# Performance work log

Hardware: AMD Instinct MI355X
Metric: run time of the kernel (lower is better)

The kernel has to match this reference:

```python
import jax, jax.numpy as jnp
import numpy as np

B, L, V, DM, NL, NH, DH, FF, K = 32, 128, 30522, 768, 12, 12, 64, 3072, 9
T = L - 1  # [CLS] stripped


def setup_inputs() -> dict:
    key = jax.random.key(0)
    ks = jax.random.split(key, 24)
    w = lambda k, s: jax.random.normal(k, s, jnp.float32) * 0.02
    u = lambda k, s: jax.random.uniform(k, s, jnp.float32, -0.1, 0.1)  # torchcrf init
    return dict(
        input_ids=jax.random.randint(ks[0], (B, L), 0, V, jnp.int32),
        attention_mask=jnp.ones((B, L), jnp.int32),
        token_type_ids=jnp.zeros((B, L), jnp.int32),
        y_true=jax.random.randint(ks[1], (B, T), 0, K, jnp.int32),
        word_emb=w(ks[2], (V, DM)), pos_emb=w(ks[3], (L, DM)), type_emb=w(ks[4], (2, DM)),
        emb_g=jnp.ones((DM,), jnp.float32), emb_b=jnp.zeros((DM,), jnp.float32),
        Wq=w(ks[5], (NL, DM, DM)), bq=jnp.zeros((NL, DM), jnp.float32),
        Wk=w(ks[6], (NL, DM, DM)), bk=jnp.zeros((NL, DM), jnp.float32),
        Wv=w(ks[7], (NL, DM, DM)), bv=jnp.zeros((NL, DM), jnp.float32),
        Wo=w(ks[8], (NL, DM, DM)), bo=jnp.zeros((NL, DM), jnp.float32),
        ln1_g=jnp.ones((NL, DM), jnp.float32), ln1_b=jnp.zeros((NL, DM), jnp.float32),
        W1=w(ks[9], (NL, DM, FF)), b1=jnp.zeros((NL, FF), jnp.float32),
        W2=w(ks[10], (NL, FF, DM)), b2=jnp.zeros((NL, DM), jnp.float32),
        ln2_g=jnp.ones((NL, DM), jnp.float32), ln2_b=jnp.zeros((NL, DM), jnp.float32),
        head_W=w(ks[11], (DM, K)), head_b=jnp.zeros((K,), jnp.float32),
        crf_start=u(ks[12], (K,)), crf_end=u(ks[13], (K,)), crf_trans=u(ks[14], (K, K)),
    )


def _ln(x, g, b):
    m = jnp.mean(x, -1, keepdims=True)
    v = jnp.var(x, -1, keepdims=True)
    return (x - m) * jax.lax.rsqrt(v + 1e-12) * g + b


def reference(input_ids, attention_mask, token_type_ids, y_true, word_emb, pos_emb,
              type_emb, emb_g, emb_b, Wq, bq, Wk, bk, Wv, bv, Wo, bo, ln1_g, ln1_b,
              W1, b1, W2, b2, ln2_g, ln2_b, head_W, head_b, crf_start, crf_end, crf_trans):
    # ----- BERT-base encoder -----
    x = word_emb[input_ids] + pos_emb[None, :, :] + type_emb[token_type_ids]
    x = _ln(x, emb_g, emb_b)
    bias = (1.0 - attention_mask.astype(jnp.float32))[:, None, None, :] * -1e9
    scale = 1.0 / jnp.sqrt(jnp.float32(DH))

    def layer(h, p):
        wq, bq_, wk, bk_, wv, bv_, wo, bo_, g1, gb1, w1, b1_, w2, b2_, g2, gb2 = p
        q = (h @ wq + bq_).reshape(B, L, NH, DH)
        k = (h @ wk + bk_).reshape(B, L, NH, DH)
        v = (h @ wv + bv_).reshape(B, L, NH, DH)
        s = jnp.einsum('bqhd,bkhd->bhqk', q, k) * scale + bias
        a = jax.nn.softmax(s, axis=-1)
        ctx = jnp.einsum('bhqk,bkhd->bqhd', a, v).reshape(B, L, DM)
        h = _ln(h + ctx @ wo + bo_, g1, gb1)
        f = jax.nn.gelu(h @ w1 + b1_, approximate=False)
        h = _ln(h + f @ w2 + b2_, g2, gb2)
        return h, None

    x, _ = jax.lax.scan(layer, x, (Wq, bq, Wk, bk, Wv, bv, Wo, bo, ln1_g, ln1_b,
                                   W1, b1, W2, b2, ln2_g, ln2_b))
    # strip [CLS], linear head -> emissions [B,T,K]
    em = x[:, 1:, :] @ head_W + head_b
    mask = attention_mask[:, 1:].astype(bool)  # [B,T]

    # ----- CRF (torchcrf semantics, batch_first) -----
    em_tm = jnp.transpose(em, (1, 0, 2))  # [T,B,K]
    mask_tm = mask.T                      # [T,B]
    tags_tm = y_true.T                    # [T,B]
    mf = mask_tm.astype(em.dtype)

    # numerator: score of gold path
    emit = jnp.take_along_axis(em_tm, tags_tm[:, :, None], -1)[..., 0]  # [T,B]
    tr = crf_trans[tags_tm[:-1], tags_tm[1:]]                           # [T-1,B]
    num = crf_start[tags_tm[0]] + emit[0] + jnp.sum((tr + emit[1:]) * mf[1:], 0)
    last_idx = jnp.sum(mask.astype(jnp.int32), 1) - 1
    last_tag = jnp.take_along_axis(y_true, last_idx[:, None], 1)[:, 0]
    num = num + crf_end[last_tag]

    # denominator: forward algorithm
    def fstep(alpha, inp):
        e, m = inp
        nxt = jax.scipy.special.logsumexp(alpha[:, :, None] + crf_trans[None], axis=1) + e
        return jnp.where(m[:, None], nxt, alpha), None

    alpha, _ = jax.lax.scan(fstep, crf_start + em_tm[0], (em_tm[1:], mask_tm[1:]))
    Z = jax.scipy.special.logsumexp(alpha + crf_end, -1)
    llh = jnp.mean(num - Z)  # reduction='mean'

    # Viterbi decode
    def vstep(score, inp):
        e, m = inp
        cand = score[:, :, None] + crf_trans[None]   # [B,K_prev,K_next]
        nxt = jnp.max(cand, 1) + e
        return jnp.where(m[:, None], nxt, score), jnp.argmax(cand, 1)

    score, hist = jax.lax.scan(vstep, crf_start + em_tm[0], (em_tm[1:], mask_tm[1:]))
    last = jnp.argmax(score + crf_end, -1)  # [B]

    def bstep(tag, inp):
        h, m = inp
        prev = jnp.take_along_axis(h, tag[:, None], 1)[:, 0]
        return jnp.where(m, prev, tag), tag

    first, ys = jax.lax.scan(bstep, last, (hist, mask_tm[1:]), reverse=True)
    decoded = jnp.concatenate([first[None], ys], 0).T  # [B,T]
    return llh, decoded
```

## Files before the change

kernel.cpp:

```cpp
#include <hip/hip_runtime.h>
#include <math.h>


#define Bz 32
#define Lz 128
#define DMz 768
#define NLz 12
#define NHz 12
#define DHz 64
#define FFz 3072
#define Kz 9
#define Tz 127
#define RR (Bz * Lz)
#define QKVP 2304

typedef float f32x4v __attribute__((ext_vector_type(4)));
typedef _Float16 f16x8v __attribute__((ext_vector_type(8)));

__device__ __forceinline__ float wred(float v) {
#pragma unroll
    for (int o = 32; o > 0; o >>= 1) v += __shfl_down(v, o, 64);
    return v;
}

__global__ void sentinel_k(float* out) {
    if (threadIdx.x == 0) out[0] = 123456.0f;
}

__global__ __launch_bounds__(256) void embed_ln_k(
    const int* __restrict__ ids, const int* __restrict__ tts,
    const float* __restrict__ we, const float* __restrict__ pe, const float* __restrict__ te,
    const float* __restrict__ g, const float* __restrict__ bb, float* __restrict__ X)
{
    int r = blockIdx.x;
    int pos = r & (Lz - 1);
    int tid = threadIdx.x;
    int id = ids[r], tt = tts[r];
    __shared__ float buf[DMz];
    __shared__ float sa[4], sb[4];
    float s = 0.f, s2 = 0.f;
    for (int d = tid; d < DMz; d += 256) {
        float v = we[(size_t)id * DMz + d] + pe[pos * DMz + d] + te[tt * DMz + d];
        buf[d] = v; s += v; s2 += v * v;
    }
    float w1 = wred(s), w2 = wred(s2);
    if ((tid & 63) == 0) { sa[tid >> 6] = w1; sb[tid >> 6] = w2; }
    __syncthreads();
    float S = sa[0] + sa[1] + sa[2] + sa[3];
    float S2 = sb[0] + sb[1] + sb[2] + sb[3];
    float mean = S * (1.f / DMz);
    float var = S2 * (1.f / DMz) - mean * mean;
    float inv = rsqrtf(var + 1e-12f);
    for (int d = tid; d < DMz; d += 256)
        X[(size_t)r * DMz + d] = (buf[d] - mean) * inv * g[d] + bb[d];
}

__global__ __launch_bounds__(256) void addln_k(
    float* __restrict__ X, const float* __restrict__ Y,
    const float* __restrict__ g, const float* __restrict__ bb)
{
    int r = blockIdx.x;
    int tid = threadIdx.x;
    __shared__ float buf[DMz];
    __shared__ float sa[4], sb2[4];
    size_t base = (size_t)r * DMz;
    float s = 0.f, s2 = 0.f;
    for (int d = tid; d < DMz; d += 256) {
        float v = X[base + d] + Y[base + d];
        buf[d] = v; s += v; s2 += v * v;
    }
    float w1 = wred(s), w2 = wred(s2);
    if ((tid & 63) == 0) { sa[tid >> 6] = w1; sb2[tid >> 6] = w2; }
    __syncthreads();
    float S = sa[0] + sa[1] + sa[2] + sa[3];
    float S2 = sb2[0] + sb2[1] + sb2[2] + sb2[3];
    float mean = S * (1.f / DMz);
    float var = S2 * (1.f / DMz) - mean * mean;
    float inv = rsqrtf(var + 1e-12f);
    for (int d = tid; d < DMz; d += 256)
        X[base + d] = (buf[d] - mean) * inv * g[d] + bb[d];
}

__global__ __launch_bounds__(256) void bbfill_k(
    const float* __restrict__ bq, const float* __restrict__ bk,
    const float* __restrict__ bv, float* __restrict__ BB)
{
    int i = blockIdx.x * 256 + threadIdx.x;
    if (i >= NLz * QKVP) return;
    int l = i / QKVP, j = i - l * QKVP;
    float v;
    if (j < 768) v = bq[l * 768 + j];
    else if (j < 1536) v = bk[l * 768 + j - 768];
    else v = bv[l * 768 + j - 1536];
    BB[i] = v;
}

__global__ __launch_bounds__(256) void wt_k(
    const float* __restrict__ W, int ldw, int Kt, int Nt,
    _Float16* __restrict__ oh, _Float16* __restrict__ ol, int orow0, int opitch)
{
    (void)Kt; (void)Nt;
    __shared__ float LS[64][65];
    int n0 = blockIdx.x * 64, k0 = blockIdx.y * 64;
    int t = threadIdx.x;
    int kr = t >> 2, nc = (t & 3) * 16;
    const float* wp = W + (size_t)(k0 + kr) * ldw + n0 + nc;
    float4 v0 = *(const float4*)(wp);
    float4 v1 = *(const float4*)(wp + 4);
    float4 v2 = *(const float4*)(wp + 8);
    float4 v3 = *(const float4*)(wp + 12);
    float* lsp = &LS[kr][nc];
    lsp[0] = v0.x; lsp[1] = v0.y; lsp[2] = v0.z; lsp[3] = v0.w;
    lsp[4] = v1.x; lsp[5] = v1.y; lsp[6] = v1.z; lsp[7] = v1.w;
    lsp[8] = v2.x; lsp[9] = v2.y; lsp[10] = v2.z; lsp[11] = v2.w;
    lsp[12] = v3.x; lsp[13] = v3.y; lsp[14] = v3.z; lsp[15] = v3.w;
    __syncthreads();
    int n = t >> 2, kq = (t & 3) * 16;
    __align__(16) _Float16 hh[16], ll[16];
#pragma unroll
    for (int j = 0; j < 16; j++) {
        float v = LS[kq + j][n];
        _Float16 h = (_Float16)v;
        hh[j] = h;
        ll[j] = (_Float16)(v - (float)h);
    }
    size_t ob = (size_t)(orow0 + n0 + n) * opitch + k0 + kq;
    *(uint4*)&oh[ob]     = *(uint4*)&hh[0];
    *(uint4*)&oh[ob + 8] = *(uint4*)&hh[8];
    *(uint4*)&ol[ob]     = *(uint4*)&ll[0];
    *(uint4*)&ol[ob + 8] = *(uint4*)&ll[8];
}

__global__ __launch_bounds__(256) void gemm_mx_k(
    const float* __restrict__ A, int lda,
    const _Float16* __restrict__ Wh, const _Float16* __restrict__ Wl,
    const float* __restrict__ bias, float* __restrict__ C, int ldc,
    int Kd, int act, int accum)
{
    __shared__ _Float16 Ahs[128][40];
    __shared__ _Float16 Als[128][40];
    __shared__ _Float16 Bhs[128][40];
    __shared__ _Float16 Bls[128][40];
    int tid = threadIdx.x;
    int lane = tid & 63, wid = tid >> 6;
    int wr = wid >> 1, wc = wid & 1;
    int row0 = blockIdx.y * 128, col0 = blockIdx.x * 128;
    int sr = tid >> 1;
    int sk = (tid & 1) << 4;

    const float* ap = A + (size_t)(row0 + sr) * lda + sk;
    const _Float16* whp = Wh + (size_t)(col0 + sr) * Kd + sk;
    const _Float16* wlp = Wl + (size_t)(col0 + sr) * Kd + sk;

    f32x4v acc[4][4];
#pragma unroll
    for (int i = 0; i < 4; i++)
#pragma unroll
        for (int j = 0; j < 4; j++) acc[i][j] = (f32x4v)0.f;

    __align__(16) float av[16];
    uint4 bhr0, bhr1, blr0, blr1;
#define LOADAB(ko) do { \
        *(float4*)&av[0]  = *(const float4*)(ap + (ko)); \
        *(float4*)&av[4]  = *(const float4*)(ap + (ko) + 4); \
        *(float4*)&av[8]  = *(const float4*)(ap + (ko) + 8); \
        *(float4*)&av[12] = *(const float4*)(ap + (ko) + 12); \
        bhr0 = *(const uint4*)(whp + (ko)); \
        bhr1 = *(const uint4*)(whp + (ko) + 8); \
        blr0 = *(const uint4*)(wlp + (ko)); \
        blr1 = *(const uint4*)(wlp + (ko) + 8); \
    } while (0)

    LOADAB(0);
    int nk = Kd >> 5;
    int arow = wr * 64 + (lane & 15);
    int bcol = wc * 64 + (lane & 15);
    int kb = (lane >> 4) << 3;

    for (int kt = 0; kt < nk; ++kt) {
        __syncthreads();
        {
            __align__(16) _Float16 hh[16], ll[16];
#pragma unroll
            for (int i = 0; i < 16; i++) {
                _Float16 h = (_Float16)av[i];
                hh[i] = h;
                ll[i] = (_Float16)(av[i] - (float)h);
            }
            *(uint4*)&Ahs[sr][sk]     = *(uint4*)&hh[0];
            *(uint4*)&Ahs[sr][sk + 8] = *(uint4*)&hh[8];
            *(uint4*)&Als[sr][sk]     = *(uint4*)&ll[0];
            *(uint4*)&Als[sr][sk + 8] = *(uint4*)&ll[8];
            *(uint4*)&Bhs[sr][sk]     = bhr0;
            *(uint4*)&Bhs[sr][sk + 8] = bhr1;
            *(uint4*)&Bls[sr][sk]     = blr0;
            *(uint4*)&Bls[sr][sk + 8] = blr1;
        }
        __syncthreads();
        if (kt + 1 < nk) { LOADAB((kt + 1) << 5); }

        f16x8v afh[4], afl[4];
#pragma unroll
        for (int mi = 0; mi < 4; mi++) {
            afh[mi] = *(const f16x8v*)&Ahs[arow + mi * 16][kb];
            afl[mi] = *(const f16x8v*)&Als[arow + mi * 16][kb];
        }
#pragma unroll
        for (int ni = 0; ni < 4; ni++) {
            f16x8v bfh = *(const f16x8v*)&Bhs[bcol + ni * 16][kb];
            f16x8v bfl = *(const f16x8v*)&Bls[bcol + ni * 16][kb];
#pragma unroll
            for (int mi = 0; mi < 4; mi++) {
                acc[mi][ni] = __builtin_amdgcn_mfma_f32_16x16x32_f16(afh[mi], bfh, acc[mi][ni], 0, 0, 0);
                acc[mi][ni] = __builtin_amdgcn_mfma_f32_16x16x32_f16(afh[mi], bfl, acc[mi][ni], 0, 0, 0);
                acc[mi][ni] = __builtin_amdgcn_mfma_f32_16x16x32_f16(afl[mi], bfh, acc[mi][ni], 0, 0, 0);
            }
        }
    }
#undef LOADAB

    int rb2 = (lane >> 4) << 2;
    int cb = lane & 15;
#pragma unroll
    for (int mi = 0; mi < 4; mi++) {
#pragma unroll
        for (int ni = 0; ni < 4; ni++) {
            int cc = col0 + wc * 64 + ni * 16 + cb;
            float bv = bias ? bias[cc] : 0.f;
#pragma unroll
            for (int r = 0; r < 4; r++) {
                int rr = row0 + wr * 64 + mi * 16 + rb2 + r;
                float v = acc[mi][ni][r] + bv;
                if (act == 1) v = 0.5f * v * (1.0f + erff(v * 0.70710678118f));
                size_t o = (size_t)rr * ldc + cc;
                if (accum) v += C[o];
                C[o] = v;
            }
        }
    }
}

__global__ __launch_bounds__(128) void attn_k(
    const float* __restrict__ QKV, const int* __restrict__ am, float* __restrict__ CTX)
{
    int bh = blockIdx.x;
    int b = bh / NHz, h = bh - b * NHz;
    __shared__ float Ks[64][DHz];
    __shared__ float Vs[64][DHz];
    int tid = threadIdx.x;
    float qreg[DHz];
    {
        const float* qp = QKV + (size_t)(b * Lz + tid) * QKVP + h * DHz;
#pragma unroll
        for (int d = 0; d < DHz; d++) qreg[d] = qp[d];
    }
    float m = -INFINITY, l = 0.f;
    float ctx[DHz];
#pragma unroll
    for (int d = 0; d < DHz; d++) ctx[d] = 0.f;
    for (int kc = 0; kc < Lz; kc += 64) {
        __syncthreads();
        for (int i = tid; i < 64 * DHz; i += 128) {
            int kk = i >> 6, d = i & 63;
            size_t base = (size_t)(b * Lz + kc + kk) * QKVP + h * DHz + d;
            Ks[kk][d] = QKV[base + 768];
            Vs[kk][d] = QKV[base + 1536];
        }
        __syncthreads();
        for (int k = 0; k < 64; k++) {
            float s = 0.f;
#pragma unroll
            for (int d = 0; d < DHz; d++) s = fmaf(qreg[d], Ks[k][d], s);
            s = s * 0.125f + (1.0f - (float)am[b * Lz + kc + k]) * -1e9f;
            float nm = fmaxf(m, s);
            float alpha = __expf(m - nm);
            float p = __expf(s - nm);
            l = l * alpha + p;
#pragma unroll
            for (int d = 0; d < DHz; d++) ctx[d] = ctx[d] * alpha + p * Vs[k][d];
            m = nm;
        }
    }
    float inv = 1.0f / l;
    float* cp = CTX + (size_t)(b * Lz + tid) * DMz + h * DHz;
#pragma unroll
    for (int d = 0; d < DHz; d++) cp[d] = ctx[d] * inv;
}

__global__ __launch_bounds__(64) void head_k(
    const float* __restrict__ X, const float* __restrict__ hW, const float* __restrict__ hb,
    float* __restrict__ EM)
{
    int rt = blockIdx.x;
    int b = rt / Tz, t = rt - b * Tz;
    int lane = threadIdx.x;
    const float* xp = X + (size_t)(b * Lz + t + 1) * DMz;
    float acc[Kz];
#pragma unroll
    for (int k = 0; k < Kz; k++) acc[k] = 0.f;
    for (int d = lane; d < DMz; d += 64) {
        float xv = xp[d];
#pragma unroll
        for (int k = 0; k < Kz; k++) acc[k] = fmaf(xv, hW[d * Kz + k], acc[k]);
    }
#pragma unroll
    for (int k = 0; k < Kz; k++) acc[k] = wred(acc[k]);
    if (lane == 0) {
#pragma unroll
        for (int k = 0; k < Kz; k++) EM[(size_t)rt * Kz + k] = acc[k] + hb[k];
    }
}

__global__ __launch_bounds__(128) void crf_k(
    const float* __restrict__ EM, const int* __restrict__ yt, const int* __restrict__ am,
    const float* __restrict__ cs, const float* __restrict__ ce, const float* __restrict__ ctr,
    int* __restrict__ hist, float* __restrict__ out)
{
    __shared__ float tr[Kz * Kz], st[Kz], en[Kz], nums[Bz], Zs[Bz];
    int tid = threadIdx.x;
    if (tid < Kz * Kz) tr[tid] = ctr[tid];
    if (tid < Kz) { st[tid] = cs[tid]; en[tid] = ce[tid]; }
    __syncthreads();
    if (tid < Bz) {
        int b = tid;
        const float* em = EM + (size_t)b * Tz * Kz;
        const int* y = yt + b * Tz;
        const int* mr = am + b * Lz;
        float num = st[y[0]] + em[y[0]];
        for (int t = 1; t < Tz; t++) {
            float mf = (mr[t + 1] != 0) ? 1.f : 0.f;
            num += (tr[y[t - 1] * Kz + y[t]] + em[t * Kz + y[t]]) * mf;
        }
        int lastidx = -1;
        for (int t = 0; t < Tz; t++) lastidx += (mr[t + 1] != 0) ? 1 : 0;
        num += en[y[lastidx]];
        nums[b] = num;
        float alpha[Kz];
#pragma unroll
        for (int j = 0; j < Kz; j++) alpha[j] = st[j] + em[j];
        for (int t = 1; t < Tz; t++) {
            bool mm = mr[t + 1] != 0;
            float nxt[Kz];
            for (int j = 0; j < Kz; j++) {
                float mx = -1e30f;
                for (int i = 0; i < Kz; i++) mx = fmaxf(mx, alpha[i] + tr[i * Kz + j]);
                float sm = 0.f;
                for (int i = 0; i < Kz; i++) sm += expf(alpha[i] + tr[i * Kz + j] - mx);
                nxt[j] = mx + logf(sm) + em[t * Kz + j];
            }
            if (mm) { for (int j = 0; j < Kz; j++) alpha[j] = nxt[j]; }
        }
        float mx = -1e30f;
        for (int j = 0; j < Kz; j++) mx = fmaxf(mx, alpha[j] + en[j]);
        float sm = 0.f;
        for (int j = 0; j < Kz; j++) sm += expf(alpha[j] + en[j] - mx);
        Zs[b] = mx + logf(sm);
    } else if (tid >= 64 && tid < 64 + Bz) {
        int b = tid - 64;
        const float* em = EM + (size_t)b * Tz * Kz;
        const int* mr = am + b * Lz;
        int* hb = hist + (size_t)b * (Tz - 1) * Kz;
        float sc[Kz];
#pragma unroll
        for (int j = 0; j < Kz; j++) sc[j] = st[j] + em[j];
        for (int t = 1; t < Tz; t++) {
            bool mm = mr[t + 1] != 0;
            float nxt[Kz]; int arg[Kz];
            for (int j = 0; j < Kz; j++) {
                float best = -1e30f; int bi = 0;
                for (int i = 0; i < Kz; i++) {
                    float v = sc[i] + tr[i * Kz + j];
                    if (v > best) { best = v; bi = i; }
                }
                nxt[j] = best + em[t * Kz + j]; arg[j] = bi;
            }
            for (int j = 0; j < Kz; j++) hb[(size_t)(t - 1) * Kz + j] = arg[j];
            if (mm) { for (int j = 0; j < Kz; j++) sc[j] = nxt[j]; }
        }
        float best = -1e30f; int last = 0;
        for (int j = 0; j < Kz; j++) { float v = sc[j] + en[j]; if (v > best) { best = v; last = j; } }
        int tag = last;
        for (int t = Tz - 2; t >= 0; t--) {
            out[1 + b * Tz + (t + 1)] = (float)tag;
            int prev = hb[(size_t)t * Kz + tag];
            if (mr[t + 2] != 0) tag = prev;
        }
        out[1 + b * Tz] = (float)tag;
    }
    __syncthreads();
    if (tid == 0) {
        float s = 0.f;
        for (int b = 0; b < Bz; b++) s += nums[b] - Zs[b];
        out[0] = s * (1.0f / Bz);
    }
}

extern "C" void kernel_launch(void* const* d_in, const int* in_sizes, int n_in,
                              void* d_out, int out_size, void* d_ws, size_t ws_size,
                              hipStream_t stream)
{
    (void)in_sizes; (void)n_in; (void)out_size; (void)ws_size;
    const int* ids    = (const int*)d_in[0];
    const int* amask  = (const int*)d_in[1];
    const int* tts    = (const int*)d_in[2];
    const int* ytrue  = (const int*)d_in[3];
    const float* we   = (const float*)d_in[4];
    const float* pe   = (const float*)d_in[5];
    const float* te   = (const float*)d_in[6];
    const float* eg   = (const float*)d_in[7];
    const float* eb   = (const float*)d_in[8];
    const float* Wq   = (const float*)d_in[9];
    const float* bq   = (const float*)d_in[10];
    const float* Wk   = (const float*)d_in[11];
    const float* bk   = (const float*)d_in[12];
    const float* Wv   = (const float*)d_in[13];
    const float* bv   = (const float*)d_in[14];
    const float* Wo   = (const float*)d_in[15];
    const float* bo   = (const float*)d_in[16];
    const float* ln1g = (const float*)d_in[17];
    const float* ln1b = (const float*)d_in[18];
    const float* W1   = (const float*)d_in[19];
    const float* b1   = (const float*)d_in[20];
    const float* W2   = (const float*)d_in[21];
    const float* b2   = (const float*)d_in[22];
    const float* ln2g = (const float*)d_in[23];
    const float* ln2b = (const float*)d_in[24];
    const float* hW   = (const float*)d_in[25];
    const float* hb   = (const float*)d_in[26];
    const float* cs   = (const float*)d_in[27];
    const float* ce   = (const float*)d_in[28];
    const float* ctr  = (const float*)d_in[29];

    float* ws = (float*)d_ws;
    size_t RDM = (size_t)RR * DMz;
    float* X  = ws;
    float* B1 = X  + RDM;
    float* B2 = B1 + RDM;
    float* B3 = B2 + RDM;
    float* B4 = B3 + RDM;
    float* F  = B2;
    float* EM = B4 + RDM;
    int*  HIST = (int*)(EM + (size_t)Bz * Tz * Kz);
    float* BB  = (float*)(HIST + (size_t)Bz * (Tz - 1) * Kz);

    (void)hipGetLastError();
    sentinel_k<<<1, 64, 0, stream>>>((float*)d_out);
    embed_ln_k<<<RR, 256, 0, stream>>>(ids, tts, we, pe, te, eg, eb, X);
    bbfill_k<<<(NLz * QKVP + 255) / 256, 256, 0, stream>>>(bq, bk, bv, BB);

    for (int l = 0; l < NLz; l++) {
        size_t wofs = (size_t)l * DMz * DMz;
        _Float16* wt4h = (_Float16*)B4;
        _Float16* wt4l = wt4h + (size_t)QKVP * DMz;
        wt_k<<<dim3(12, 12), 256, 0, stream>>>(Wq + wofs, DMz, DMz, DMz, wt4h, wt4l, 0, DMz);
        wt_k<<<dim3(12, 12), 256, 0, stream>>>(Wk + wofs, DMz, DMz, DMz, wt4h, wt4l, 768, DMz);
        wt_k<<<dim3(12, 12), 256, 0, stream>>>(Wv + wofs, DMz, DMz, DMz, wt4h, wt4l, 1536, DMz);
        gemm_mx_k<<<dim3(18, 32), 256, 0, stream>>>(X, DMz, wt4h, wt4l, BB + l * QKVP,
                                                    B1, QKVP, DMz, 0, 0);
        attn_k<<<Bz * NHz, 128, 0, stream>>>(B1, amask, B4);
        _Float16* wt1h = (_Float16*)B1;
        _Float16* wt1l = wt1h + (size_t)DMz * DMz;
        wt_k<<<dim3(12, 12), 256, 0, stream>>>(Wo + wofs, DMz, DMz, DMz, wt1h, wt1l, 0, DMz);
        gemm_mx_k<<<dim3(6, 32), 256, 0, stream>>>(B4, DMz, wt1h, wt1l, bo + l * DMz,
                                                   B2, DMz, DMz, 0, 0);
        addln_k<<<RR, 256, 0, stream>>>(X, B2, ln1g + l * DMz, ln1b + l * DMz);
        const float* W1l = W1 + (size_t)l * DMz * FFz;
        const float* W2l = W2 + (size_t)l * FFz * DMz;
        const float* b1l = b1 + (size_t)l * FFz;
        _Float16* wtfh = (_Float16*)B1;
        _Float16* wtfl = wtfh + (size_t)1536 * DMz;
        wt_k<<<dim3(24, 12), 256, 0, stream>>>(W1l, FFz, DMz, 1536, wtfh, wtfl, 0, DMz);
        gemm_mx_k<<<dim3(12, 32), 256, 0, stream>>>(X, DMz, wtfh, wtfl, b1l,
                                                    F, 1536, DMz, 1, 0);
        wt_k<<<dim3(12, 24), 256, 0, stream>>>(W2l, DMz, 1536, DMz, wtfh, wtfl, 0, 1536);
        gemm_mx_k<<<dim3(6, 32), 256, 0, stream>>>(F, 1536, wtfh, wtfl, b2 + l * DMz,
                                                   B4, DMz, 1536, 0, 0);
        wt_k<<<dim3(24, 12), 256, 0, stream>>>(W1l + 1536, FFz, DMz, 1536, wtfh, wtfl, 0, DMz);
        gemm_mx_k<<<dim3(12, 32), 256, 0, stream>>>(X, DMz, wtfh, wtfl, b1l + 1536,
                                                    F, 1536, DMz, 1, 0);
        wt_k<<<dim3(12, 24), 256, 0, stream>>>(W2l + (size_t)1536 * DMz, DMz, 1536, DMz,
                                               wtfh, wtfl, 0, 1536);
        gemm_mx_k<<<dim3(6, 32), 256, 0, stream>>>(F, 1536, wtfh, wtfl, nullptr,
                                                   B4, DMz, 1536, 0, 1);
        addln_k<<<RR, 256, 0, stream>>>(X, B4, ln2g + l * DMz, ln2b + l * DMz);
    }
    head_k<<<Bz * Tz, 64, 0, stream>>>(X, hW, hb, EM);
    crf_k<<<1, 128, 0, stream>>>(EM, ytrue, amask, cs, ce, ctr, HIST, (float*)d_out);

    if (hipGetLastError() != hipSuccess) {
        hipMemsetAsync(d_out, 0xFF, 4, stream);
    }
}
```

Measured before the change: 7.084 ms.

## Pre-swizzle weight tiles into MFMA fragment order, load via LDS DMA, parallelize CRF

The weight transpose kernel now writes the fp16 hi/lo split weights as contiguous 128x32 tiles already arranged in MFMA fragment order. The GEMM streams those tiles straight into double-buffered shared memory with global_load_lds and stores A in fragment order as well, which removes padded row-major LDS tiles and register staging for B. The CRF kernel now runs one block per batch element, with lanes holding tags, shuffle-based forward and Viterbi recurrences, backpointers in shared memory and a separate reduction kernel. In exchange the GEMM uses more LDS (a second B buffer) and the code relies on a custom tile layout.

Result: no change. 7.029 ms (-0.8%).

```diff
diff --git a/kernel.cpp b/kernel.cpp
--- a/kernel.cpp
+++ b/kernel.cpp
@@ -23,6 +23,12 @@
     return v;
 }
 
+__device__ __forceinline__ void gload16(const void* g, void* l) {
+    __builtin_amdgcn_global_load_lds(
+        (const __attribute__((address_space(1))) void*)g,
+        (__attribute__((address_space(3))) void*)l, 16, 0, 0);
+}
+
 __global__ void sentinel_k(float* out) {
     if (threadIdx.x == 0) out[0] = 123456.0f;
 }
@@ -96,61 +102,63 @@
 }
 
 __global__ __launch_bounds__(256) void wt_k(
-    const float* __restrict__ W, int ldw, int Kt, int Nt,
-    _Float16* __restrict__ oh, _Float16* __restrict__ ol, int orow0, int opitch)
-{
-    (void)Kt; (void)Nt;
-    __shared__ float LS[64][65];
-    int n0 = blockIdx.x * 64, k0 = blockIdx.y * 64;
+    const float* __restrict__ W, int ldw, _Float16* __restrict__ WT,
+    int nkt, int nb0)
+{
+    __shared__ float LS[32][132];
+    int nb = blockIdx.x, kt = blockIdx.y;
     int t = threadIdx.x;
-    int kr = t >> 2, nc = (t & 3) * 16;
-    const float* wp = W + (size_t)(k0 + kr) * ldw + n0 + nc;
-    float4 v0 = *(const float4*)(wp);
-    float4 v1 = *(const float4*)(wp + 4);
-    float4 v2 = *(const float4*)(wp + 8);
-    float4 v3 = *(const float4*)(wp + 12);
-    float* lsp = &LS[kr][nc];
-    lsp[0] = v0.x; lsp[1] = v0.y; lsp[2] = v0.z; lsp[3] = v0.w;
-    lsp[4] = v1.x; lsp[5] = v1.y; lsp[6] = v1.z; lsp[7] = v1.w;
-    lsp[8] = v2.x; lsp[9] = v2.y; lsp[10] = v2.z; lsp[11] = v2.w;
-    lsp[12] = v3.x; lsp[13] = v3.y; lsp[14] = v3.z; lsp[15] = v3.w;
+    int kr = t >> 3, nc = (t & 7) << 4;
+    const float* wp = W + (size_t)(kt * 32 + kr) * ldw + nb * 128 + nc;
+    float4 a = *(const float4*)wp;
+    float4 b = *(const float4*)(wp + 4);
+    float4 c4 = *(const float4*)(wp + 8);
+    float4 d = *(const float4*)(wp + 12);
+    float* q = &LS[kr][nc];
+    q[0]=a.x;q[1]=a.y;q[2]=a.z;q[3]=a.w;
+    q[4]=b.x;q[5]=b.y;q[6]=b.z;q[7]=b.w;
+    q[8]=c4.x;q[9]=c4.y;q[10]=c4.z;q[11]=c4.w;
+    q[12]=d.x;q[13]=d.y;q[14]=d.z;q[15]=d.w;
     __syncthreads();
-    int n = t >> 2, kq = (t & 3) * 16;
-    __align__(16) _Float16 hh[16], ll[16];
-#pragma unroll
-    for (int j = 0; j < 16; j++) {
-        float v = LS[kq + j][n];
-        _Float16 h = (_Float16)v;
-        hh[j] = h;
-        ll[j] = (_Float16)(v - (float)h);
-    }
-    size_t ob = (size_t)(orow0 + n0 + n) * opitch + k0 + kq;
-    *(uint4*)&oh[ob]     = *(uint4*)&hh[0];
-    *(uint4*)&oh[ob + 8] = *(uint4*)&hh[8];
-    *(uint4*)&ol[ob]     = *(uint4*)&ll[0];
-    *(uint4*)&ol[ob + 8] = *(uint4*)&ll[8];
+    int lane = t & 63, w = t >> 6;
+    _Float16* outb = WT + ((size_t)(nb0 + nb) * nkt + kt) * 8192;
+#pragma unroll
+    for (int j = 0; j < 4; j++) {
+        int cc = w * 4 + j;
+        int wc = cc >> 3, p = (cc >> 2) & 1, ni = cc & 3;
+        int n = wc * 64 + ni * 16 + (lane & 15);
+        int k8 = (lane >> 4) << 3;
+        __align__(16) _Float16 bf[8];
+#pragma unroll
+        for (int jj = 0; jj < 8; jj++) {
+            float v = LS[k8 + jj][n];
+            _Float16 h = (_Float16)v;
+            bf[jj] = p ? (_Float16)(v - (float)h) : h;
+        }
+        *(uint4*)&outb[(size_t)(cc * 64 + lane) * 8] = *(uint4*)&bf[0];
+    }
 }
 
 __global__ __launch_bounds__(256) void gemm_mx_k(
     const float* __restrict__ A, int lda,
-    const _Float16* __restrict__ Wh, const _Float16* __restrict__ Wl,
+    const _Float16* __restrict__ WT,
     const float* __restrict__ bias, float* __restrict__ C, int ldc,
     int Kd, int act, int accum)
 {
-    __shared__ _Float16 Ahs[128][40];
-    __shared__ _Float16 Als[128][40];
-    __shared__ _Float16 Bhs[128][40];
-    __shared__ _Float16 Bls[128][40];
+    __shared__ __align__(16) _Float16 Asm[8192];
+    __shared__ __align__(16) _Float16 Bsm[2][8192];
     int tid = threadIdx.x;
-    int lane = tid & 63, wid = tid >> 6;
-    int wr = wid >> 1, wc = wid & 1;
+    int lane = tid & 63, w = tid >> 6;
+    int wr = w >> 1, wc = w & 1;
     int row0 = blockIdx.y * 128, col0 = blockIdx.x * 128;
+    int nk = Kd >> 5;
     int sr = tid >> 1;
     int sk = (tid & 1) << 4;
-
+    int swr = sr >> 6, smi = (sr >> 4) & 3, srr = sr & 15;
+    int o0 = (tid & 1) << 1;
     const float* ap = A + (size_t)(row0 + sr) * lda + sk;
-    const _Float16* whp = Wh + (size_t)(col0 + sr) * Kd + sk;
-    const _Float16* wlp = Wl + (size_t)(col0 + sr) * Kd + sk;
+    const _Float16* wtb = WT + (size_t)((col0 >> 7) * nk) * 8192 + (w << 11) + (lane << 3);
+    int ldst = (w << 11) + (lane << 3);
 
     f32x4v acc[4][4];
 #pragma unroll
@@ -159,23 +167,21 @@
         for (int j = 0; j < 4; j++) acc[i][j] = (f32x4v)0.f;
 
     __align__(16) float av[16];
-    uint4 bhr0, bhr1, blr0, blr1;
-#define LOADAB(ko) do { \
-        *(float4*)&av[0]  = *(const float4*)(ap + (ko)); \
-        *(float4*)&av[4]  = *(const float4*)(ap + (ko) + 4); \
-        *(float4*)&av[8]  = *(const float4*)(ap + (ko) + 8); \
-        *(float4*)&av[12] = *(const float4*)(ap + (ko) + 12); \
-        bhr0 = *(const uint4*)(whp + (ko)); \
-        bhr1 = *(const uint4*)(whp + (ko) + 8); \
-        blr0 = *(const uint4*)(wlp + (ko)); \
-        blr1 = *(const uint4*)(wlp + (ko) + 8); \
+#define LOADA(kt) do { \
+        const float* _p = ap + ((kt) << 5); \
+        *(float4*)&av[0]  = *(const float4*)(_p); \
+        *(float4*)&av[4]  = *(const float4*)(_p + 4); \
+        *(float4*)&av[8]  = *(const float4*)(_p + 8); \
+        *(float4*)&av[12] = *(const float4*)(_p + 12); \
     } while (0)
 
-    LOADAB(0);
-    int nk = Kd >> 5;
-    int arow = wr * 64 + (lane & 15);
-    int bcol = wc * 64 + (lane & 15);
-    int kb = (lane >> 4) << 3;
+    LOADA(0);
+#pragma unroll
+    for (int j = 0; j < 4; j++)
+        gload16(wtb + (j << 9), &Bsm[0][ldst + (j << 9)]);
+
+    int abase_hi = ((swr << 3) + smi) * 512;
+    int abase_lo = abase_hi + 2048;
 
     for (int kt = 0; kt < nk; ++kt) {
         __syncthreads();
@@ -187,28 +193,31 @@
                 hh[i] = h;
                 ll[i] = (_Float16)(av[i] - (float)h);
             }
-            *(uint4*)&Ahs[sr][sk]     = *(uint4*)&hh[0];
-            *(uint4*)&Ahs[sr][sk + 8] = *(uint4*)&hh[8];
-            *(uint4*)&Als[sr][sk]     = *(uint4*)&ll[0];
-            *(uint4*)&Als[sr][sk + 8] = *(uint4*)&ll[8];
-            *(uint4*)&Bhs[sr][sk]     = bhr0;
-            *(uint4*)&Bhs[sr][sk + 8] = bhr1;
-            *(uint4*)&Bls[sr][sk]     = blr0;
-            *(uint4*)&Bls[sr][sk + 8] = blr1;
+            *(uint4*)&Asm[abase_hi + ((o0    ) * 16 + srr) * 8] = *(uint4*)&hh[0];
+            *(uint4*)&Asm[abase_hi + ((o0 + 1) * 16 + srr) * 8] = *(uint4*)&hh[8];
+            *(uint4*)&Asm[abase_lo + ((o0    ) * 16 + srr) * 8] = *(uint4*)&ll[0];
+            *(uint4*)&Asm[abase_lo + ((o0 + 1) * 16 + srr) * 8] = *(uint4*)&ll[8];
         }
         __syncthreads();
-        if (kt + 1 < nk) { LOADAB((kt + 1) << 5); }
-
+        if (kt + 1 < nk) {
+            const _Float16* ts = wtb + (size_t)(kt + 1) * 8192;
+            _Float16* db = &Bsm[(kt + 1) & 1][ldst];
+#pragma unroll
+            for (int j = 0; j < 4; j++)
+                gload16(ts + (j << 9), db + (j << 9));
+            LOADA(kt + 1);
+        }
+        const _Float16* Bc = &Bsm[kt & 1][0];
         f16x8v afh[4], afl[4];
 #pragma unroll
         for (int mi = 0; mi < 4; mi++) {
-            afh[mi] = *(const f16x8v*)&Ahs[arow + mi * 16][kb];
-            afl[mi] = *(const f16x8v*)&Als[arow + mi * 16][kb];
+            afh[mi] = *(const f16x8v*)&Asm[(((wr << 1) + 0) * 4 + mi) * 512 + (lane << 3)];
+            afl[mi] = *(const f16x8v*)&Asm[(((wr << 1) + 1) * 4 + mi) * 512 + (lane << 3)];
         }
 #pragma unroll
         for (int ni = 0; ni < 4; ni++) {
-            f16x8v bfh = *(const f16x8v*)&Bhs[bcol + ni * 16][kb];
-            f16x8v bfl = *(const f16x8v*)&Bls[bcol + ni * 16][kb];
+            f16x8v bfh = *(const f16x8v*)&Bc[(((wc << 1) + 0) * 4 + ni) * 512 + (lane << 3)];
+            f16x8v bfl = *(const f16x8v*)&Bc[(((wc << 1) + 1) * 4 + ni) * 512 + (lane << 3)];
 #pragma unroll
             for (int mi = 0; mi < 4; mi++) {
                 acc[mi][ni] = __builtin_amdgcn_mfma_f32_16x16x32_f16(afh[mi], bfh, acc[mi][ni], 0, 0, 0);
@@ -217,7 +226,7 @@
             }
         }
     }
-#undef LOADAB
+#undef LOADA
 
     int rb2 = (lane >> 4) << 2;
     int cb = lane & 15;
@@ -314,85 +323,103 @@
 __global__ __launch_bounds__(128) void crf_k(
     const float* __restrict__ EM, const int* __restrict__ yt, const int* __restrict__ am,
     const float* __restrict__ cs, const float* __restrict__ ce, const float* __restrict__ ctr,
-    int* __restrict__ hist, float* __restrict__ out)
-{
-    __shared__ float tr[Kz * Kz], st[Kz], en[Kz], nums[Bz], Zs[Bz];
+    float* __restrict__ part, float* __restrict__ out)
+{
+    int b = blockIdx.x;
     int tid = threadIdx.x;
-    if (tid < Kz * Kz) tr[tid] = ctr[tid];
-    if (tid < Kz) { st[tid] = cs[tid]; en[tid] = ce[tid]; }
+    int lane = tid & 63, wv = tid >> 6;
+    __shared__ float em_s[Tz * Kz];
+    __shared__ float tr_s[Kz * Kz], st_s[Kz], en_s[Kz];
+    __shared__ int y_s[Tz], mk_s[Lz];
+    __shared__ int hist_s[(Tz - 1) * Kz];
+    const float* em = EM + (size_t)b * Tz * Kz;
+    for (int i = tid; i < Tz * Kz; i += 128) em_s[i] = em[i];
+    if (tid < Kz * Kz) tr_s[tid] = ctr[tid];
+    if (tid < Kz) { st_s[tid] = cs[tid]; en_s[tid] = ce[tid]; }
+    for (int i = tid; i < Tz; i += 128) y_s[i] = yt[b * Tz + i];
+    for (int i = tid; i < Lz; i += 128) mk_s[i] = am[b * Lz + i];
     __syncthreads();
-    if (tid < Bz) {
-        int b = tid;
-        const float* em = EM + (size_t)b * Tz * Kz;
-        const int* y = yt + b * Tz;
-        const int* mr = am + b * Lz;
-        float num = st[y[0]] + em[y[0]];
+    int jj = (lane < Kz) ? lane : 0;
+    if (wv == 0) {
+        float np = 0.f;
+        for (int t = 1 + lane; t < Tz; t += 64)
+            if (mk_s[t + 1] != 0)
+                np += tr_s[y_s[t - 1] * Kz + y_s[t]] + em_s[t * Kz + y_s[t]];
+        float cnt = 0.f;
+        for (int t = lane; t < Tz; t += 64) cnt += (mk_s[t + 1] != 0) ? 1.f : 0.f;
+        np = wred(np);
+        cnt = wred(cnt);
+        float trc[Kz];
+#pragma unroll
+        for (int i = 0; i < Kz; i++) trc[i] = tr_s[i * Kz + jj];
+        float alpha = (lane < Kz) ? st_s[lane] + em_s[lane] : 0.f;
         for (int t = 1; t < Tz; t++) {
-            float mf = (mr[t + 1] != 0) ? 1.f : 0.f;
-            num += (tr[y[t - 1] * Kz + y[t]] + em[t * Kz + y[t]]) * mf;
-        }
-        int lastidx = -1;
-        for (int t = 0; t < Tz; t++) lastidx += (mr[t + 1] != 0) ? 1 : 0;
-        num += en[y[lastidx]];
-        nums[b] = num;
-        float alpha[Kz];
-#pragma unroll
-        for (int j = 0; j < Kz; j++) alpha[j] = st[j] + em[j];
+            float vv[Kz], mx = -1e30f;
+#pragma unroll
+            for (int i = 0; i < Kz; i++) {
+                float ai = __shfl(alpha, i, 64);
+                vv[i] = ai + trc[i];
+                mx = fmaxf(mx, vv[i]);
+            }
+            float sm = 0.f;
+#pragma unroll
+            for (int i = 0; i < Kz; i++) sm += __expf(vv[i] - mx);
+            float nx = mx + __logf(sm) + em_s[t * Kz + jj];
+            if (mk_s[t + 1] != 0) alpha = nx;
+        }
+        float zvl = alpha + en_s[jj];
+        float zz[Kz], zmx = -1e30f, zsm = 0.f;
+#pragma unroll
+        for (int i = 0; i < Kz; i++) {
+            zz[i] = __shfl(zvl, i, 64);
+            zmx = fmaxf(zmx, zz[i]);
+        }
+#pragma unroll
+        for (int i = 0; i < Kz; i++) zsm += __expf(zz[i] - zmx);
+        if (lane == 0) {
+            int lastidx = (int)cnt - 1;
+            float num = st_s[y_s[0]] + em_s[y_s[0]] + np + en_s[y_s[lastidx]];
+            part[b] = num - (zmx + __logf(zsm));
+        }
+    } else {
+        float trc[Kz];
+#pragma unroll
+        for (int i = 0; i < Kz; i++) trc[i] = tr_s[i * Kz + jj];
+        float sc = (lane < Kz) ? st_s[lane] + em_s[lane] : -1e30f;
         for (int t = 1; t < Tz; t++) {
-            bool mm = mr[t + 1] != 0;
-            float nxt[Kz];
-            for (int j = 0; j < Kz; j++) {
-                float mx = -1e30f;
-                for (int i = 0; i < Kz; i++) mx = fmaxf(mx, alpha[i] + tr[i * Kz + j]);
-                float sm = 0.f;
-                for (int i = 0; i < Kz; i++) sm += expf(alpha[i] + tr[i * Kz + j] - mx);
-                nxt[j] = mx + logf(sm) + em[t * Kz + j];
+            float best = -1e30f; int bi = 0;
+#pragma unroll
+            for (int i = 0; i < Kz; i++) {
+                float v = __shfl(sc, i, 64) + trc[i];
+                if (v > best) { best = v; bi = i; }
             }
-            if (mm) { for (int j = 0; j < Kz; j++) alpha[j] = nxt[j]; }
-        }
-        float mx = -1e30f;
-        for (int j = 0; j < Kz; j++) mx = fmaxf(mx, alpha[j] + en[j]);
-        float sm = 0.f;
-        for (int j = 0; j < Kz; j++) sm += expf(alpha[j] + en[j] - mx);
-        Zs[b] = mx + logf(sm);
-    } else if (tid >= 64 && tid < 64 + Bz) {
-        int b = tid - 64;
-        const float* em = EM + (size_t)b * Tz * Kz;
-        const int* mr = am + b * Lz;
-        int* hb = hist + (size_t)b * (Tz - 1) * Kz;
-        float sc[Kz];
-#pragma unroll
-        for (int j = 0; j < Kz; j++) sc[j] = st[j] + em[j];
-        for (int t = 1; t < Tz; t++) {
-            bool mm = mr[t + 1] != 0;
-            float nxt[Kz]; int arg[Kz];
-            for (int j = 0; j < Kz; j++) {
-                float best = -1e30f; int bi = 0;
-                for (int i = 0; i < Kz; i++) {
-                    float v = sc[i] + tr[i * Kz + j];
-                    if (v > best) { best = v; bi = i; }
-                }
-                nxt[j] = best + em[t * Kz + j]; arg[j] = bi;
+            if (lane < Kz) hist_s[(t - 1) * Kz + lane] = bi;
+            float nx = best + em_s[t * Kz + jj];
+            if (mk_s[t + 1] != 0) sc = nx;
+        }
+        float bestv = -1e30f; int last = 0;
+#pragma unroll
+        for (int j = 0; j < Kz; j++) {
+            float v = __shfl(sc, j, 64) + en_s[j];
+            if (v > bestv) { bestv = v; last = j; }
+        }
+        if (lane == 0) {
+            int tag = last;
+            for (int t = Tz - 2; t >= 0; t--) {
+                out[1 + b * Tz + (t + 1)] = (float)tag;
+                int prev = hist_s[t * Kz + tag];
+                if (mk_s[t + 2] != 0) tag = prev;
             }
-            for (int j = 0; j < Kz; j++) hb[(size_t)(t - 1) * Kz + j] = arg[j];
-            if (mm) { for (int j = 0; j < Kz; j++) sc[j] = nxt[j]; }
-        }
-        float best = -1e30f; int last = 0;
-        for (int j = 0; j < Kz; j++) { float v = sc[j] + en[j]; if (v > best) { best = v; last = j; } }
-        int tag = last;
-        for (int t = Tz - 2; t >= 0; t--) {
-            out[1 + b * Tz + (t + 1)] = (float)tag;
-            int prev = hb[(size_t)t * Kz + tag];
-            if (mr[t + 2] != 0) tag = prev;
-        }
-        out[1 + b * Tz] = (float)tag;
-    }
-    __syncthreads();
-    if (tid == 0) {
-        float s = 0.f;
-        for (int b = 0; b < Bz; b++) s += nums[b] - Zs[b];
-        out[0] = s * (1.0f / Bz);
-    }
+            out[1 + b * Tz] = (float)tag;
+        }
+    }
+}
+
+__global__ __launch_bounds__(64) void crffin_k(const float* __restrict__ part, float* __restrict__ out) {
+    int lane = threadIdx.x;
+    float v = (lane < Bz) ? part[lane] : 0.f;
+    v = wred(v);
+    if (lane == 0) out[0] = v * (1.0f / Bz);
 }
 
 extern "C" void kernel_launch(void* const* d_in, const int* in_sizes, int n_in,
@@ -440,8 +467,8 @@
     float* B4 = B3 + RDM;
     float* F  = B2;
     float* EM = B4 + RDM;
-    int*  HIST = (int*)(EM + (size_t)Bz * Tz * Kz);
-    float* BB  = (float*)(HIST + (size_t)Bz * (Tz - 1) * Kz);
+    float* PART = EM + (size_t)Bz * Tz * Kz;
+    float* BB   = PART + 64;
 
     (void)hipGetLastError();
     sentinel_k<<<1, 64, 0, stream>>>((float*)d_out);
@@ -450,42 +477,38 @@
 
     for (int l = 0; l < NLz; l++) {
         size_t wofs = (size_t)l * DMz * DMz;
-        _Float16* wt4h = (_Float16*)B4;
-        _Float16* wt4l = wt4h + (size_t)QKVP * DMz;
-        wt_k<<<dim3(12, 12), 256, 0, stream>>>(Wq + wofs, DMz, DMz, DMz, wt4h, wt4l, 0, DMz);
-        wt_k<<<dim3(12, 12), 256, 0, stream>>>(Wk + wofs, DMz, DMz, DMz, wt4h, wt4l, 768, DMz);
-        wt_k<<<dim3(12, 12), 256, 0, stream>>>(Wv + wofs, DMz, DMz, DMz, wt4h, wt4l, 1536, DMz);
-        gemm_mx_k<<<dim3(18, 32), 256, 0, stream>>>(X, DMz, wt4h, wt4l, BB + l * QKVP,
+        _Float16* wt4 = (_Float16*)B4;
+        wt_k<<<dim3(6, 24), 256, 0, stream>>>(Wq + wofs, DMz, wt4, 24, 0);
+        wt_k<<<dim3(6, 24), 256, 0, stream>>>(Wk + wofs, DMz, wt4, 24, 6);
+        wt_k<<<dim3(6, 24), 256, 0, stream>>>(Wv + wofs, DMz, wt4, 24, 12);
+        gemm_mx_k<<<dim3(18, 32), 256, 0, stream>>>(X, DMz, wt4, BB + l * QKVP,
                                                     B1, QKVP, DMz, 0, 0);
         attn_k<<<Bz * NHz, 128, 0, stream>>>(B1, amask, B4);
-        _Float16* wt1h = (_Float16*)B1;
-        _Float16* wt1l = wt1h + (size_t)DMz * DMz;
-        wt_k<<<dim3(12, 12), 256, 0, stream>>>(Wo + wofs, DMz, DMz, DMz, wt1h, wt1l, 0, DMz);
-        gemm_mx_k<<<dim3(6, 32), 256, 0, stream>>>(B4, DMz, wt1h, wt1l, bo + l * DMz,
+        _Float16* wt1 = (_Float16*)B1;
+        wt_k<<<dim3(6, 24), 256, 0, stream>>>(Wo + wofs, DMz, wt1, 24, 0);
+        gemm_mx_k<<<dim3(6, 32), 256, 0, stream>>>(B4, DMz, wt1, bo + l * DMz,
                                                    B2, DMz, DMz, 0, 0);
         addln_k<<<RR, 256, 0, stream>>>(X, B2, ln1g + l * DMz, ln1b + l * DMz);
         const float* W1l = W1 + (size_t)l * DMz * FFz;
         const float* W2l = W2 + (size_t)l * FFz * DMz;
         const float* b1l = b1 + (size_t)l * FFz;
-        _Float16* wtfh = (_Float16*)B1;
-        _Float16* wtfl = wtfh + (size_t)1536 * DMz;
-        wt_k<<<dim3(24, 12), 256, 0, stream>>>(W1l, FFz, DMz, 1536, wtfh, wtfl, 0, DMz);
-        gemm_mx_k<<<dim3(12, 32), 256, 0, stream>>>(X, DMz, wtfh, wtfl, b1l,
+        wt_k<<<dim3(12, 24), 256, 0, stream>>>(W1l, FFz, wt1, 24, 0);
+        gemm_mx_k<<<dim3(12, 32), 256, 0, stream>>>(X, DMz, wt1, b1l,
                                                     F, 1536, DMz, 1, 0);
-        wt_k<<<dim3(12, 24), 256, 0, stream>>>(W2l, DMz, 1536, DMz, wtfh, wtfl, 0, 1536);
-        gemm_mx_k<<<dim3(6, 32), 256, 0, stream>>>(F, 1536, wtfh, wtfl, b2 + l * DMz,
+        wt_k<<<dim3(6, 48), 256, 0, stream>>>(W2l, DMz, wt1, 48, 0);
+        gemm_mx_k<<<dim3(6, 32), 256, 0, stream>>>(F, 1536, wt1, b2 + l * DMz,
                                                    B4, DMz, 1536, 0, 0);
-        wt_k<<<dim3(24, 12), 256, 0, stream>>>(W1l + 1536, FFz, DMz, 1536, wtfh, wtfl, 0, DMz);
-        gemm_mx_k<<<dim3(12, 32), 256, 0, stream>>>(X, DMz, wtfh, wtfl, b1l + 1536,
+        wt_k<<<dim3(12, 24), 256, 0, stream>>>(W1l + 1536, FFz, wt1, 24, 0);
+        gemm_mx_k<<<dim3(12, 32), 256, 0, stream>>>(X, DMz, wt1, b1l + 1536,
                                                     F, 1536, DMz, 1, 0);
-        wt_k<<<dim3(12, 24), 256, 0, stream>>>(W2l + (size_t)1536 * DMz, DMz, 1536, DMz,
-                                               wtfh, wtfl, 0, 1536);
-        gemm_mx_k<<<dim3(6, 32), 256, 0, stream>>>(F, 1536, wtfh, wtfl, nullptr,
+        wt_k<<<dim3(6, 48), 256, 0, stream>>>(W2l + (size_t)1536 * DMz, DMz, wt1, 48, 0);
+        gemm_mx_k<<<dim3(6, 32), 256, 0, stream>>>(F, 1536, wt1, nullptr,
                                                    B4, DMz, 1536, 0, 1);
         addln_k<<<RR, 256, 0, stream>>>(X, B4, ln2g + l * DMz, ln2b + l * DMz);
     }
     head_k<<<Bz * Tz, 64, 0, stream>>>(X, hW, hb, EM);
-    crf_k<<<1, 128, 0, stream>>>(EM, ytrue, amask, cs, ce, ctr, HIST, (float*)d_out);
+    crf_k<<<Bz, 128, 0, stream>>>(EM, ytrue, amask, cs, ce, ctr, PART, (float*)d_out);
+    crffin_k<<<1, 64, 0, stream>>>(PART, (float*)d_out);
 
     if (hipGetLastError() != hipSuccess) {
         hipMemsetAsync(d_out, 0xFF, 4, stream);
```
